# Performance work log

Hardware: AMD Instinct MI355X
Metric: run time of the kernel (lower is better)

## Reference

```python
import jax, jax.numpy as jnp
import numpy as np

N, C, S, NS = 65536, 64, 8, 16  # points, channels, share_planes, nsample
CS = C // S
EPS = 1e-5


def _bn(x, g, b, m, v):
    # BatchNorm1d in eval mode over the last (channel) axis
    return (x - m) * (g * jax.lax.rsqrt(v + EPS)) + b


def setup_inputs() -> dict:
    key = jax.random.key(0)
    ks = jax.random.split(key, 32)
    rn = lambda k, s: jax.random.normal(k, s, jnp.float32)
    un = lambda k, s: jax.random.uniform(k, s, jnp.float32, 0.5, 1.5)
    return {
        "p": rn(ks[0], (N, 3)),
        "x": rn(ks[1], (N, C)),
        "idx": jax.random.randint(ks[2], (N, NS), 0, N),
        "Wq": rn(ks[3], (C, C)) * 0.1, "bq": rn(ks[4], (C,)) * 0.1,
        "Wk": rn(ks[5], (C, C)) * 0.1, "bk": rn(ks[6], (C,)) * 0.1,
        "Wv": rn(ks[7], (C, C)) * 0.1, "bv": rn(ks[8], (C,)) * 0.1,
        "Wp1": rn(ks[9], (3, 3)) * 0.3, "bp1": rn(ks[10], (3,)) * 0.1,
        "pg": un(ks[11], (3,)), "pb": rn(ks[12], (3,)) * 0.1,
        "pm": rn(ks[13], (3,)) * 0.1, "pv": un(ks[14], (3,)),
        "Wp2": rn(ks[15], (C, 3)) * 0.3, "bp2": rn(ks[16], (C,)) * 0.1,
        "wg1": un(ks[17], (C,)), "wb1": rn(ks[18], (C,)) * 0.1,
        "wm1": rn(ks[19], (C,)) * 0.1, "wv1": un(ks[20], (C,)),
        "Ww1": rn(ks[21], (CS, C)) * 0.1, "bw1": rn(ks[22], (CS,)) * 0.1,
        "wg2": un(ks[23], (CS,)), "wb2": rn(ks[24], (CS,)) * 0.1,
        "wm2": rn(ks[25], (CS,)) * 0.1, "wv2": un(ks[26], (CS,)),
        "Ww2": rn(ks[27], (CS, CS)) * 0.1, "bw2": rn(ks[28], (CS,)) * 0.1,
    }


def _forward(p, x, idx, Wq, bq, Wk, bk, Wv, bv, Wp1, bp1, pg, pb, pm, pv,
             Wp2, bp2, wg1, wb1, wm1, wv1, Ww1, bw1, wg2, wb2, wm2, wv2, Ww2, bw2):
    xq = x @ Wq.T + bq                      # [N, C]
    xk = (x @ Wk.T + bk)[idx]               # [N, NS, C] neighbor gather
    xv = (x @ Wv.T + bv)[idx]               # [N, NS, C]
    pr = p[idx] - p[:, None, :]             # [N, NS, 3] relative coords (queryandgroup use_xyz)
    # linear_p: Conv1d(3,3,1) -> BN(3) -> ReLU -> Conv1d(3,C,1) (pointwise)
    t = jax.nn.relu(_bn(pr @ Wp1.T + bp1, pg, pb, pm, pv))
    pr = t @ Wp2.T + bp2                    # [N, NS, C] positional encoding
    # out_planes // mid_planes == 1, so p_r.view(...).sum(2) is identity
    w = xk - xq[:, None, :] + pr            # [N, NS, C] relation
    # linear_w: BN(C) -> ReLU -> Conv(C,C/S) -> BN(C/S) -> ReLU -> Conv(C/S,C/S)
    w = jax.nn.relu(_bn(w, wg1, wb1, wm1, wv1))
    w = jax.nn.relu(_bn(w @ Ww1.T + bw1, wg2, wb2, wm2, wv2))
    w = w @ Ww2.T + bw2                     # [N, NS, C//S]
    w = jax.nn.softmax(w, axis=1)           # softmax over the neighbor axis
    out = ((xv + pr).reshape(N, NS, S, CS) * w[:, :, None, :]).sum(axis=1)
    return out.reshape(N, C)


def reference(p, x, idx, Wq, bq, Wk, bk, Wv, bv, Wp1, bp1, pg, pb, pm, pv,
              Wp2, bp2, wg1, wb1, wm1, wv1, Ww1, bw1, wg2, wb2, wm2, wv2, Ww2, bw2):
    return _forward(p, x, idx, Wq, bq, Wk, bk, Wv, bv, Wp1, bp1, pg, pb, pm, pv,
                    Wp2, bp2, wg1, wb1, wm1, wv1, Ww1, bw1, wg2, wb2, wm2, wv2, Ww2, bw2)
```

## Files before the change

### kernel.cpp

```cpp
#include <hip/hip_runtime.h>

#define NPTS 65536
#define EPSV 1e-5f

typedef unsigned int uint_t;
typedef unsigned short ushort_t;
typedef __attribute__((ext_vector_type(8))) short short8;
typedef __attribute__((ext_vector_type(4))) float float4v;

union U8 { uint4 u; short8 s; };

__device__ __forceinline__ ushort_t f2bf(float f) {
    unsigned u = __float_as_uint(f);
    unsigned r = (u + 0x7fffu + ((u >> 16) & 1u)) >> 16;
    return (ushort_t)r;
}

__device__ __forceinline__ uint_t pkrn(uint_t lo, uint_t hi) {
    return ((lo + 0x8000u) >> 16) | ((hi + 0x8000u) & 0xffff0000u);
}

__device__ __forceinline__ short8 packG(const float* p8) {
    float4 a = *(const float4*)p8;
    float4 b = *(const float4*)(p8 + 4);
    U8 c;
    c.u.x = pkrn(__float_as_uint(a.x), __float_as_uint(a.y));
    c.u.y = pkrn(__float_as_uint(a.z), __float_as_uint(a.w));
    c.u.z = pkrn(__float_as_uint(b.x), __float_as_uint(b.y));
    c.u.w = pkrn(__float_as_uint(b.z), __float_as_uint(b.w));
    return c.s;
}

#define WBAR() do { asm volatile("s_waitcnt lgkmcnt(0)" ::: "memory"); \
                    __builtin_amdgcn_wave_barrier(); } while (0)

__global__ __launch_bounds__(256) void k_qkv(
    const float* __restrict__ x,
    const float* __restrict__ Wq, const float* __restrict__ bq,
    const float* __restrict__ Wk, const float* __restrict__ bk,
    const float* __restrict__ Wv, const float* __restrict__ bv,
    float* __restrict__ xq, uint_t* __restrict__ kvp)
{
    __shared__ __align__(16) ushort_t sA[64 * 72];
    __shared__ __align__(16) ushort_t sB[192 * 72];

    const int tid  = threadIdx.x;
    const int lane = tid & 63;
    const int w    = tid >> 6;
    const int n0   = blockIdx.x * 64;

    const float4* xg = (const float4*)(x + (size_t)n0 * 64);
#pragma unroll
    for (int i = 0; i < 4; ++i) {
        int f = i * 256 + tid;
        float4 v = xg[f];
        int r = f >> 4, c4 = f & 15;
        uint2 pk;
        pk.x = (uint_t)f2bf(v.x) | ((uint_t)f2bf(v.y) << 16);
        pk.y = (uint_t)f2bf(v.z) | ((uint_t)f2bf(v.w) << 16);
        *(uint2*)(sA + r * 72 + c4 * 4) = pk;
    }
#pragma unroll
    for (int i = 0; i < 12; ++i) {
        const float* src = (i < 4) ? Wq : (i < 8) ? Wk : Wv;
        int f = i * 256 + tid;
        int r = f >> 4, c4 = f & 15;
        float4 v = ((const float4*)src)[(i & 3) * 256 + tid];
        uint2 pk;
        pk.x = (uint_t)f2bf(v.x) | ((uint_t)f2bf(v.y) << 16);
        pk.y = (uint_t)f2bf(v.z) | ((uint_t)f2bf(v.w) << 16);
        *(uint2*)(sB + r * 72 + c4 * 4) = pk;
    }
    __syncthreads();

    const int quad = lane >> 4;
    const int cn   = lane & 15;
    const int mrow = (w << 4) + cn;

    short8 a0 = *(const short8*)(sA + mrow * 72 + quad * 8);
    short8 a1 = *(const short8*)(sA + mrow * 72 + 32 + quad * 8);

    float4v acc[12];
#pragma unroll
    for (int t = 0; t < 12; ++t) {
        const int brow = t * 16 + cn;
        short8 b0 = *(const short8*)(sB + brow * 72 + quad * 8);
        short8 b1 = *(const short8*)(sB + brow * 72 + 32 + quad * 8);
        float4v c = {0.f, 0.f, 0.f, 0.f};
        c = __builtin_amdgcn_mfma_f32_16x16x32_bf16(a0, b0, c, 0, 0, 0);
        c = __builtin_amdgcn_mfma_f32_16x16x32_bf16(a1, b1, c, 0, 0, 0);
        acc[t] = c;
    }

    const int orow = n0 + (w << 4) + quad * 4;
#pragma unroll
    for (int t = 0; t < 4; ++t) {
        int o = t * 16 + cn;
        float bqv = bq[o], bkv = bk[o], bvv = bv[o];
        float4v aq = acc[t], ak = acc[4 + t], av = acc[8 + t];
#pragma unroll
        for (int r = 0; r < 4; ++r) {
            size_t base = (size_t)(orow + r) * 64 + o;
            xq[base]  = aq[r] + bqv;
            kvp[base] = (uint_t)f2bf(ak[r] + bkv) | ((uint_t)f2bf(av[r] + bvv) << 16);
        }
    }
}

__global__ __launch_bounds__(256, 4) void k_attn(
    const float* __restrict__ p, const int* __restrict__ idx,
    const float* __restrict__ xq, const uint_t* __restrict__ kvp,
    const float* __restrict__ Wp1, const float* __restrict__ bp1,
    const float* __restrict__ pg, const float* __restrict__ pb,
    const float* __restrict__ pm, const float* __restrict__ pv,
    const float* __restrict__ Wp2, const float* __restrict__ bp2,
    const float* __restrict__ wg1, const float* __restrict__ wb1,
    const float* __restrict__ wm1, const float* __restrict__ wv1,
    const float* __restrict__ Ww1, const float* __restrict__ bw1,
    const float* __restrict__ wg2, const float* __restrict__ wb2,
    const float* __restrict__ wm2, const float* __restrict__ wv2,
    const float* __restrict__ Ww2, const float* __restrict__ bw2,
    float* __restrict__ out)
{
    __shared__ __align__(16) ushort_t swr[4][16 * 72];
    __shared__ __align__(16) ushort_t shl[4][16 * 40];
    __shared__ __align__(16) float    swt[4][4 * 16 * 4];
    __shared__ __align__(16) float    swg[4][8 * 20];

    const int tid   = threadIdx.x;
    const int wid   = __builtin_amdgcn_readfirstlane(tid >> 6);
    const int lane  = tid & 63;
    const int nbase = blockIdx.x * 16 + wid * 4;

    ushort_t* wrelh = swr[wid];
    ushort_t* hLh   = shl[wid];
    float*    stt   = swt[wid];
    float*    wgt   = swg[wid];

    const int cm  = lane & 15;
    const int q   = lane >> 4;
    const int m8  = lane & 7;
    const int cmc = cm & 7;
    const bool colv = cm < 8;

    const int* idxr = idx + (size_t)nbase * 16;

    uint_t ga[16], gb[16];
    auto issueF = [&](int pt, uint_t (&dst)[16]) {
#pragma unroll
        for (int j = 0; j < 16; ++j) {
            int id = __builtin_amdgcn_readfirstlane(idxr[pt * 16 + j]);
            dst[j] = kvp[(size_t)id * 64 + lane];
        }
    };

    issueF(0, ga);
    issueF(1, gb);

    {
        uint_t* hz = (uint_t*)hLh;
        for (int i = lane; i < 16 * 20; i += 64) hz[i] = 0u;
    }

    int   idv[4];
    float xqc[4];
#pragma unroll
    for (int pt = 0; pt < 4; ++pt) {
        idv[pt] = idxr[pt * 16 + cm];
        xqc[pt] = xq[(size_t)(nbase + pt) * 64 + lane];
    }
    float gpx[4], gpy[4], gpz[4];
#pragma unroll
    for (int pt = 0; pt < 4; ++pt) {
        gpx[pt] = p[idv[pt] * 3 + 0];
        gpy[pt] = p[idv[pt] * 3 + 1];
        gpz[pt] = p[idv[pt] * 3 + 2];
    }

    float w100 = Wp1[0], w101 = Wp1[1], w102 = Wp1[2];
    float w110 = Wp1[3], w111 = Wp1[4], w112 = Wp1[5];
    float w120 = Wp1[6], w121 = Wp1[7], w122 = Wp1[8];
    float sp0 = pg[0] * rsqrtf(pv[0] + EPSV);
    float sp1 = pg[1] * rsqrtf(pv[1] + EPSV);
    float sp2 = pg[2] * rsqrtf(pv[2] + EPSV);
    float off0 = (bp1[0] - pm[0]) * sp0 + pb[0];
    float off1 = (bp1[1] - pm[1]) * sp1 + pb[1];
    float off2 = (bp1[2] - pm[2]) * sp2 + pb[2];

    float s1 = wg1[lane] * rsqrtf(wv1[lane] + EPSV);
    float o1 = wb1[lane] - wm1[lane] * s1;
    float wp2x = Wp2[lane * 3 + 0], wp2y = Wp2[lane * 3 + 1], wp2z = Wp2[lane * 3 + 2];
    float peb = bp2[lane];

    float s2c = wg2[cmc] * rsqrtf(wv2[cmc] + EPSV);
    float o2c = wb2[cmc] - wm2[cmc] * s2c;
    float bw1c = bw1[cmc];

    short8 bf1a, bf1b, bf2;
    {
        const float* r1 = Ww1 + cmc * 64 + q * 8;
        short8 t1a = packG(r1);
        short8 t1b = packG(r1 + 32);
        short8 t2  = packG(Ww2 + cmc * 8);
        U8 z; z.u = make_uint4(0u, 0u, 0u, 0u);
        bf1a = colv ? t1a : z.s;
        bf1b = colv ? t1b : z.s;
        bf2  = (colv && q == 0) ? t2 : z.s;
    }

#pragma unroll
    for (int pt = 0; pt < 4; ++pt) {
        int n = nbase + pt;
        float pcx = p[n * 3 + 0], pcy = p[n * 3 + 1], pcz = p[n * 3 + 2];
        float prx = gpx[pt] - pcx, pry = gpy[pt] - pcy, prz = gpz[pt] - pcz;
        float t0 = fmaxf(fmaf(fmaf(prx, w100, fmaf(pry, w101, prz * w102)), sp0, off0), 0.f);
        float t1 = fmaxf(fmaf(fmaf(prx, w110, fmaf(pry, w111, prz * w112)), sp1, off1), 0.f);
        float t2 = fmaxf(fmaf(fmaf(prx, w120, fmaf(pry, w121, prz * w122)), sp2, off2), 0.f);
        if (lane < 16) {
            float4 tv = make_float4(t0, t1, t2, 0.f);
            *(float4*)(stt + (pt * 16 + cm) * 4) = tv;
        }
    }
    WBAR();

    auto computeF = [&](int pt, uint_t (&g)[16]) {
        float xqv = xqc[pt];
        float vpe[16];
#pragma unroll
        for (int j = 0; j < 16; ++j) {
            float4 t = *(const float4*)(stt + (pt * 16 + j) * 4);
            float pe = fmaf(t.x, wp2x, fmaf(t.y, wp2y, fmaf(t.z, wp2z, peb)));
            float xkj = __uint_as_float(g[j] << 16);
            float xvj = __uint_as_float(g[j] & 0xffff0000u);
            vpe[j] = xvj + pe;
            float d = (xkj - xqv) + pe;
            wrelh[j * 72 + lane] = f2bf(fmaxf(fmaf(d, s1, o1), 0.f));
        }
        WBAR();

        short8 a1a = *(const short8*)(wrelh + cm * 72 + q * 8);
        short8 a1b = *(const short8*)(wrelh + cm * 72 + 32 + q * 8);
        float4v d1 = {0.f, 0.f, 0.f, 0.f};
        d1 = __builtin_amdgcn_mfma_f32_16x16x32_bf16(a1a, bf1a, d1, 0, 0, 0);
        d1 = __builtin_amdgcn_mfma_f32_16x16x32_bf16(a1b, bf1b, d1, 0, 0, 0);
#pragma unroll
        for (int r = 0; r < 4; ++r) {
            float hv = fmaxf(fmaf(d1[r] + bw1c, s2c, o2c), 0.f);
            if (colv) hLh[(q * 4 + r) * 40 + cm] = f2bf(hv);
        }
        WBAR();

        short8 a2 = *(const short8*)(hLh + cm * 40 + q * 8);
        float4v d2 = {0.f, 0.f, 0.f, 0.f};
        d2 = __builtin_amdgcn_mfma_f32_16x16x32_bf16(a2, bf2, d2, 0, 0, 0);

        float mx = fmaxf(fmaxf(d2[0], d2[1]), fmaxf(d2[2], d2[3]));
        mx = fmaxf(mx, __shfl_xor(mx, 16));
        mx = fmaxf(mx, __shfl_xor(mx, 32));
        float e0 = __expf(d2[0] - mx), e1 = __expf(d2[1] - mx);
        float e2 = __expf(d2[2] - mx), e3 = __expf(d2[3] - mx);
        float ss = e0 + e1 + e2 + e3;
        ss += __shfl_xor(ss, 16);
        ss += __shfl_xor(ss, 32);
        float inv = 1.f / ss;
        if (colv) {
            float4 wv4 = make_float4(e0 * inv, e1 * inv, e2 * inv, e3 * inv);
            *(float4*)(wgt + cm * 20 + q * 4) = wv4;
        }
        WBAR();

        float acc = 0.f;
#pragma unroll
        for (int gq = 0; gq < 4; ++gq) {
            float4 wv4 = *(const float4*)(wgt + m8 * 20 + gq * 4);
            acc = fmaf(wv4.x, vpe[gq * 4 + 0], acc);
            acc = fmaf(wv4.y, vpe[gq * 4 + 1], acc);
            acc = fmaf(wv4.z, vpe[gq * 4 + 2], acc);
            acc = fmaf(wv4.w, vpe[gq * 4 + 3], acc);
        }
        WBAR();
        out[(size_t)(nbase + pt) * 64 + lane] = acc;
    };

    computeF(0, ga);
    issueF(2, ga);
    computeF(1, gb);
    issueF(3, gb);
    computeF(2, ga);
    computeF(3, gb);
}

extern "C" void kernel_launch(void* const* d_in, const int* in_sizes, int n_in,
                              void* d_out, int out_size, void* d_ws, size_t ws_size,
                              hipStream_t stream) {
    const float* p   = (const float*)d_in[0];
    const float* x   = (const float*)d_in[1];
    const int*   idx = (const int*)d_in[2];
    const float* Wq  = (const float*)d_in[3];  const float* bq  = (const float*)d_in[4];
    const float* Wk  = (const float*)d_in[5];  const float* bk  = (const float*)d_in[6];
    const float* Wv  = (const float*)d_in[7];  const float* bv  = (const float*)d_in[8];
    const float* Wp1 = (const float*)d_in[9];  const float* bp1 = (const float*)d_in[10];
    const float* pg  = (const float*)d_in[11]; const float* pb  = (const float*)d_in[12];
    const float* pm  = (const float*)d_in[13]; const float* pv  = (const float*)d_in[14];
    const float* Wp2 = (const float*)d_in[15]; const float* bp2 = (const float*)d_in[16];
    const float* wg1 = (const float*)d_in[17]; const float* wb1 = (const float*)d_in[18];
    const float* wm1 = (const float*)d_in[19]; const float* wv1 = (const float*)d_in[20];
    const float* Ww1 = (const float*)d_in[21]; const float* bw1 = (const float*)d_in[22];
    const float* wg2 = (const float*)d_in[23]; const float* wb2 = (const float*)d_in[24];
    const float* wm2 = (const float*)d_in[25]; const float* wv2 = (const float*)d_in[26];
    const float* Ww2 = (const float*)d_in[27]; const float* bw2 = (const float*)d_in[28];

    float*  xqw = (float*)d_ws;
    uint_t* kvw = (uint_t*)((char*)d_ws + (size_t)NPTS * 64 * sizeof(float));
    float*  outp = (float*)d_out;

    k_qkv<<<dim3(NPTS / 64), dim3(256), 0, stream>>>(x, Wq, bq, Wk, bk, Wv, bv, xqw, kvw);
    k_attn<<<dim3(NPTS / 16), dim3(256), 0, stream>>>(p, idx, xqw, kvw,
                                                      Wp1, bp1, pg, pb, pm, pv, Wp2, bp2,
                                                      wg1, wb1, wm1, wv1, Ww1, bw1,
                                                      wg2, wb2, wm2, wv2, Ww2, bw2, outp);
}
```

Measured before the change: 184.7 us.

## Interleave two points per phase with double-buffered LDS and lighter softmax

```diff
diff --git a/kernel.cpp b/kernel.cpp
--- a/kernel.cpp
+++ b/kernel.cpp
@@ -14,6 +14,9 @@
     unsigned u = __float_as_uint(f);
     unsigned r = (u + 0x7fffu + ((u >> 16) & 1u)) >> 16;
     return (ushort_t)r;
+}
+__device__ __forceinline__ ushort_t f2bfF(float f) {
+    return (ushort_t)((__float_as_uint(f) + 0x8000u) >> 16);
 }
 
 __device__ __forceinline__ uint_t pkrn(uint_t lo, uint_t hi) {
@@ -107,7 +110,7 @@
     }
 }
 
-__global__ __launch_bounds__(256, 4) void k_attn(
+__global__ __launch_bounds__(256, 3) void k_attn(
     const float* __restrict__ p, const int* __restrict__ idx,
     const float* __restrict__ xq, const uint_t* __restrict__ kvp,
     const float* __restrict__ Wp1, const float* __restrict__ bp1,
@@ -122,20 +125,17 @@
     const float* __restrict__ Ww2, const float* __restrict__ bw2,
     float* __restrict__ out)
 {
-    __shared__ __align__(16) ushort_t swr[4][16 * 72];
-    __shared__ __align__(16) ushort_t shl[4][16 * 40];
+    __shared__ __align__(16) ushort_t swr[4][2][16 * 72];
+    __shared__ __align__(16) ushort_t shl[4][2][16 * 40];
     __shared__ __align__(16) float    swt[4][4 * 16 * 4];
-    __shared__ __align__(16) float    swg[4][8 * 20];
+    __shared__ __align__(16) float    swg[4][2][8 * 20];
 
     const int tid   = threadIdx.x;
     const int wid   = __builtin_amdgcn_readfirstlane(tid >> 6);
     const int lane  = tid & 63;
     const int nbase = blockIdx.x * 16 + wid * 4;
 
-    ushort_t* wrelh = swr[wid];
-    ushort_t* hLh   = shl[wid];
-    float*    stt   = swt[wid];
-    float*    wgt   = swg[wid];
+    float* stt = swt[wid];
 
     const int cm  = lane & 15;
     const int q   = lane >> 4;
@@ -158,8 +158,9 @@
     issueF(1, gb);
 
     {
-        uint_t* hz = (uint_t*)hLh;
-        for (int i = lane; i < 16 * 20; i += 64) hz[i] = 0u;
+        uint_t* h0 = (uint_t*)&shl[wid][0][0];
+        uint_t* h1 = (uint_t*)&shl[wid][1][0];
+        for (int i = lane; i < 16 * 20; i += 64) { h0[i] = 0u; h1[i] = 0u; }
     }
 
     int   idv[4];
@@ -217,15 +218,16 @@
         float t1 = fmaxf(fmaf(fmaf(prx, w110, fmaf(pry, w111, prz * w112)), sp1, off1), 0.f);
         float t2 = fmaxf(fmaf(fmaf(prx, w120, fmaf(pry, w121, prz * w122)), sp2, off2), 0.f);
         if (lane < 16) {
-            float4 tv = make_float4(t0, t1, t2, 0.f);
-            *(float4*)(stt + (pt * 16 + cm) * 4) = tv;
-        }
-    }
-    WBAR();
-
-    auto computeF = [&](int pt, uint_t (&g)[16]) {
+            *(float4*)(stt + (pt * 16 + cm) * 4) = make_float4(t0, t1, t2, 0.f);
+        }
+    }
+    WBAR();
+
+    float vpeA[16], vpeB[16];
+
+    auto phA = [&](int pt, int par, uint_t (&g)[16], float (&vpe)[16]) {
+        ushort_t* wr = &swr[wid][par][0];
         float xqv = xqc[pt];
-        float vpe[16];
 #pragma unroll
         for (int j = 0; j < 16; ++j) {
             float4 t = *(const float4*)(stt + (pt * 16 + j) * 4);
@@ -234,60 +236,76 @@
             float xvj = __uint_as_float(g[j] & 0xffff0000u);
             vpe[j] = xvj + pe;
             float d = (xkj - xqv) + pe;
-            wrelh[j * 72 + lane] = f2bf(fmaxf(fmaf(d, s1, o1), 0.f));
-        }
-        WBAR();
-
-        short8 a1a = *(const short8*)(wrelh + cm * 72 + q * 8);
-        short8 a1b = *(const short8*)(wrelh + cm * 72 + 32 + q * 8);
+            wr[j * 72 + lane] = f2bfF(fmaxf(fmaf(d, s1, o1), 0.f));
+        }
+    };
+
+    auto phBX = [&](int par) {
+        ushort_t* wr = &swr[wid][par][0];
+        ushort_t* hh = &shl[wid][par][0];
+        short8 a1a = *(const short8*)(wr + cm * 72 + q * 8);
+        short8 a1b = *(const short8*)(wr + cm * 72 + 32 + q * 8);
         float4v d1 = {0.f, 0.f, 0.f, 0.f};
         d1 = __builtin_amdgcn_mfma_f32_16x16x32_bf16(a1a, bf1a, d1, 0, 0, 0);
         d1 = __builtin_amdgcn_mfma_f32_16x16x32_bf16(a1b, bf1b, d1, 0, 0, 0);
 #pragma unroll
         for (int r = 0; r < 4; ++r) {
             float hv = fmaxf(fmaf(d1[r] + bw1c, s2c, o2c), 0.f);
-            if (colv) hLh[(q * 4 + r) * 40 + cm] = f2bf(hv);
-        }
-        WBAR();
-
-        short8 a2 = *(const short8*)(hLh + cm * 40 + q * 8);
+            if (colv) hh[(q * 4 + r) * 40 + cm] = f2bfF(hv);
+        }
+    };
+
+    auto phBY = [&](int par) {
+        ushort_t* hh = &shl[wid][par][0];
+        float* wg = &swg[wid][par][0];
+        short8 a2 = *(const short8*)(hh + cm * 40 + q * 8);
         float4v d2 = {0.f, 0.f, 0.f, 0.f};
         d2 = __builtin_amdgcn_mfma_f32_16x16x32_bf16(a2, bf2, d2, 0, 0, 0);
-
-        float mx = fmaxf(fmaxf(d2[0], d2[1]), fmaxf(d2[2], d2[3]));
-        mx = fmaxf(mx, __shfl_xor(mx, 16));
-        mx = fmaxf(mx, __shfl_xor(mx, 32));
-        float e0 = __expf(d2[0] - mx), e1 = __expf(d2[1] - mx);
-        float e2 = __expf(d2[2] - mx), e3 = __expf(d2[3] - mx);
-        float ss = e0 + e1 + e2 + e3;
+        float e0 = __expf(d2[0]), e1 = __expf(d2[1]);
+        float e2 = __expf(d2[2]), e3 = __expf(d2[3]);
+        float ss = (e0 + e1) + (e2 + e3);
         ss += __shfl_xor(ss, 16);
         ss += __shfl_xor(ss, 32);
         float inv = 1.f / ss;
         if (colv) {
-            float4 wv4 = make_float4(e0 * inv, e1 * inv, e2 * inv, e3 * inv);
-            *(float4*)(wgt + cm * 20 + q * 4) = wv4;
-        }
-        WBAR();
-
+            *(float4*)(wg + cm * 20 + q * 4) =
+                make_float4(e0 * inv, e1 * inv, e2 * inv, e3 * inv);
+        }
+    };
+
+    auto phC = [&](int pt, int par, float (&vpe)[16]) {
+        float* wg = &swg[wid][par][0];
         float acc = 0.f;
 #pragma unroll
         for (int gq = 0; gq < 4; ++gq) {
-            float4 wv4 = *(const float4*)(wgt + m8 * 20 + gq * 4);
-            acc = fmaf(wv4.x, vpe[gq * 4 + 0], acc);
-            acc = fmaf(wv4.y, vpe[gq * 4 + 1], acc);
-            acc = fmaf(wv4.z, vpe[gq * 4 + 2], acc);
-            acc = fmaf(wv4.w, vpe[gq * 4 + 3], acc);
-        }
-        WBAR();
+            float4 w4 = *(const float4*)(wg + m8 * 20 + gq * 4);
+            acc = fmaf(w4.x, vpe[gq * 4 + 0], acc);
+            acc = fmaf(w4.y, vpe[gq * 4 + 1], acc);
+            acc = fmaf(w4.z, vpe[gq * 4 + 2], acc);
+            acc = fmaf(w4.w, vpe[gq * 4 + 3], acc);
+        }
         out[(size_t)(nbase + pt) * 64 + lane] = acc;
     };
 
-    computeF(0, ga);
+    phA(0, 0, ga, vpeA);
     issueF(2, ga);
-    computeF(1, gb);
+    phA(1, 1, gb, vpeB);
     issueF(3, gb);
-    computeF(2, ga);
-    computeF(3, gb);
+    WBAR();
+    phBX(0); phBX(1);
+    WBAR();
+    phBY(0); phBY(1);
+    WBAR();
+    phC(0, 0, vpeA); phC(1, 1, vpeB);
+
+    phA(2, 0, ga, vpeA);
+    phA(3, 1, gb, vpeB);
+    WBAR();
+    phBX(0); phBX(1);
+    WBAR();
+    phBY(0); phBY(1);
+    WBAR();
+    phC(2, 0, vpeA); phC(3, 1, vpeB);
 }
 
 extern "C" void kernel_launch(void* const* d_in, const int* in_sizes, int n_in,
```

After: 191.7 us. +3.8%, slower.
